# Kernel optimization log

Measured on AMD Instinct MI355X. Metric: run time of the kernel, lower is better.

Reference implementation:

```python
import jax, jax.numpy as jnp
import numpy as np

B, L, H, D = 1024, 32, 64, 2  # batch, lattice size, hiddenSize, inputDim (depth=1)
LOGP_FACTOR = 0.5


def setup_inputs() -> dict:
    key = jax.random.key(0)
    k0, k1, k2, k3 = jax.random.split(key, 4)
    x = jax.random.randint(k0, (B, L, L), 0, D, dtype=jnp.int32)
    # variance_scaling(fan_avg, uniform): limit = sqrt(3*scale / fan_avg)
    lim_in = float(np.sqrt(6.0 / (D + H)))
    lim_c = float(np.sqrt(3.0 / H))
    lim_out = float(np.sqrt(6.0 / (H + D)))
    Win = jax.random.uniform(k1, (D, H), jnp.float32, -lim_in, lim_in)
    Wc = jax.random.uniform(k2, (H, H), jnp.float32, -lim_c, lim_c)
    bc = jnp.zeros((H,), jnp.float32)
    Wout = jax.random.uniform(k3, (H, D), jnp.float32, -lim_out, lim_out)
    bout = jnp.zeros((D,), jnp.float32)
    return {"x": x, "Win": Win, "Wc": Wc, "bc": bc, "Wout": Wout, "bout": bout}


def reference(x, Win, Wc, bc, Wout, bout):
    Ldim = x.shape[-1]
    Hs = Wc.shape[0]
    Dd = Win.shape[0]
    # boustrophedon direction: +1 on even rows, -1 on odd rows
    dnp = np.ones(Ldim, dtype=np.int32)
    dnp[1::2] = -1
    direction = jnp.asarray(dnp)

    def flip_if(a, d):  # reverse_line: identity if d==1 else flip along axis 0
        return jnp.where(d == 1, a, jnp.flip(a, 0))

    def single(xs):  # xs: (L, L) int
        oh = jax.nn.one_hot(xs, Dd, dtype=Win.dtype)  # (L, L, D)

        def col_step(h, cin):
            cV, sH, sV = cin  # (H,), (D,), (D,)
            newR = sH + sV
            newH = jax.nn.elu((h + cV) @ Wc + bc + newR @ Win)  # RNNCell2D
            logits = jax.nn.log_softmax(newH @ Wout + bout)
            return newH, (newH, logits)

        def row_step(carry, row_in):
            prevH, prevOH = carry  # (L, H), (L, D)
            oh_row, d = row_in
            carryV = flip_if(prevH, d)
            stateV = flip_if(prevOH, d)
            stateH = jnp.concatenate(
                [jnp.zeros((1, Dd), oh.dtype), flip_if(oh_row, d)], axis=0)[:-1]
            _, (hs, logps) = jax.lax.scan(
                col_step, jnp.zeros((Hs,), Win.dtype), (carryV, stateH, stateV))
            logp_row = jnp.nan_to_num(
                jnp.sum(flip_if(logps, d) * oh_row, axis=-1), nan=-35.0)
            return (flip_if(hs, d), oh_row), logp_row

        init = (jnp.zeros((Ldim, Hs), Win.dtype), jnp.zeros((Ldim, Dd), Win.dtype))
        _, probs = jax.lax.scan(row_step, init, (oh, direction))
        return LOGP_FACTOR * jnp.sum(probs)

    return jax.vmap(single)(x)  # (B,) log-amplitudes
```

## Files before the change

### kernel.cpp

```cpp
#include <hip/hip_runtime.h>

#define LL 32
#define HH 64
#define PZS 68

typedef __attribute__((ext_vector_type(4))) float f32x4;

template <int CTRL>
__device__ __forceinline__ float dpp_add_step(float x) {
  int y = __builtin_amdgcn_update_dpp(0, __builtin_bit_cast(int, x), CTRL, 0xf, 0xf, true);
  return x + __builtin_bit_cast(float, y);
}

__device__ __forceinline__ float wave_sum64(float x) {
  x = dpp_add_step<0x111>(x);
  x = dpp_add_step<0x112>(x);
  x = dpp_add_step<0x114>(x);
  x = dpp_add_step<0x118>(x);
  x = dpp_add_step<0x142>(x);
  x = dpp_add_step<0x143>(x);
  return __builtin_bit_cast(float, __builtin_amdgcn_readlane(__builtin_bit_cast(int, x), 63));
}

__device__ __forceinline__ float rlbc(float v, int l) {
  return __builtin_bit_cast(float, __builtin_amdgcn_readlane(__builtin_bit_cast(int, v), l));
}

#define DECL_W(n) float w_##n = Wc[n * HH + lane];

#define MV4(i0, i1, i2, i3)                  \
  a0 = fmaf(rlbc(hv, i0), w_##i0, a0);       \
  a1 = fmaf(rlbc(hv, i1), w_##i1, a1);       \
  a2 = fmaf(rlbc(hv, i2), w_##i2, a2);       \
  a3 = fmaf(rlbc(hv, i3), w_##i3, a3);

#define PIN_ALL_W                                                              \
  asm volatile(""                                                              \
               : "+v"(w_0), "+v"(w_1), "+v"(w_2), "+v"(w_3), "+v"(w_4),       \
                 "+v"(w_5), "+v"(w_6), "+v"(w_7), "+v"(w_8), "+v"(w_9),       \
                 "+v"(w_10), "+v"(w_11), "+v"(w_12), "+v"(w_13), "+v"(w_14),  \
                 "+v"(w_15), "+v"(w_16), "+v"(w_17), "+v"(w_18), "+v"(w_19),  \
                 "+v"(w_20), "+v"(w_21), "+v"(w_22), "+v"(w_23), "+v"(w_24),  \
                 "+v"(w_25), "+v"(w_26), "+v"(w_27), "+v"(w_28), "+v"(w_29),  \
                 "+v"(w_30), "+v"(w_31), "+v"(w_32), "+v"(w_33), "+v"(w_34),  \
                 "+v"(w_35), "+v"(w_36), "+v"(w_37), "+v"(w_38), "+v"(w_39),  \
                 "+v"(w_40), "+v"(w_41), "+v"(w_42), "+v"(w_43), "+v"(w_44),  \
                 "+v"(w_45), "+v"(w_46), "+v"(w_47), "+v"(w_48), "+v"(w_49),  \
                 "+v"(w_50), "+v"(w_51), "+v"(w_52), "+v"(w_53), "+v"(w_54),  \
                 "+v"(w_55), "+v"(w_56), "+v"(w_57), "+v"(w_58), "+v"(w_59),  \
                 "+v"(w_60), "+v"(w_61), "+v"(w_62), "+v"(w_63), "+v"(win0),  \
                 "+v"(win1), "+v"(bcj), "+v"(dwout));

__global__ __launch_bounds__(64, 1) void rnn2d_kernel(
    const int* __restrict__ x, const float* __restrict__ Win,
    const float* __restrict__ Wc, const float* __restrict__ bc,
    const float* __restrict__ Wout, const float* __restrict__ bout,
    float* __restrict__ out) {
  const int lane = threadIdx.x;
  const int b = blockIdx.x;
  __shared__ float vrow[LL * HH];
  __shared__ float pz[LL * PZS];

  DECL_W(0)  DECL_W(1)  DECL_W(2)  DECL_W(3)  DECL_W(4)  DECL_W(5)  DECL_W(6)  DECL_W(7)
  DECL_W(8)  DECL_W(9)  DECL_W(10) DECL_W(11) DECL_W(12) DECL_W(13) DECL_W(14) DECL_W(15)
  DECL_W(16) DECL_W(17) DECL_W(18) DECL_W(19) DECL_W(20) DECL_W(21) DECL_W(22) DECL_W(23)
  DECL_W(24) DECL_W(25) DECL_W(26) DECL_W(27) DECL_W(28) DECL_W(29) DECL_W(30) DECL_W(31)
  DECL_W(32) DECL_W(33) DECL_W(34) DECL_W(35) DECL_W(36) DECL_W(37) DECL_W(38) DECL_W(39)
  DECL_W(40) DECL_W(41) DECL_W(42) DECL_W(43) DECL_W(44) DECL_W(45) DECL_W(46) DECL_W(47)
  DECL_W(48) DECL_W(49) DECL_W(50) DECL_W(51) DECL_W(52) DECL_W(53) DECL_W(54) DECL_W(55)
  DECL_W(56) DECL_W(57) DECL_W(58) DECL_W(59) DECL_W(60) DECL_W(61) DECL_W(62) DECL_W(63)

  float win0 = Win[lane];
  float win1 = Win[HH + lane];
  float bcj = bc[lane];
  float dwout = Wout[lane * 2 + 1] - Wout[lane * 2 + 0];
  const float dbout = bout[1] - bout[0];

#pragma unroll
  for (int c0 = 0; c0 < LL; ++c0) vrow[c0 * HH + lane] = 0.f;

  const int* xb = x + b * (LL * LL);
  unsigned prevmask = 0u;
  int spv = (lane < LL) ? xb[lane] : 0;
  float total_vec = 0.f;
  float hv = 0.f;

#pragma unroll 1
  for (int r = 0; r < LL; ++r) {
    const unsigned curmask =
        (unsigned)(__ballot(lane < LL && spv) & 0xffffffffull);
    if (r < LL - 1) spv = (lane < LL) ? xb[(r + 1) * LL + lane] : 0;

    const int odd = r & 1;
    const int d = odd ? -1 : 1;
    int c = odd ? (LL - 1) : 0;

#pragma unroll 2
    for (int k = 0; k < LL; ++k) {
      PIN_ALL_W

      const int cn = (c + d) & (LL - 1);
      const float vjn = vrow[cn * HH + lane];

      float a0 = 0.f, a1 = 0.f, a2 = 0.f, a3 = 0.f;
      MV4(0, 1, 2, 3)      MV4(4, 5, 6, 7)      MV4(8, 9, 10, 11)
      MV4(12, 13, 14, 15)  MV4(16, 17, 18, 19)  MV4(20, 21, 22, 23)
      MV4(24, 25, 26, 27)  MV4(28, 29, 30, 31)  MV4(32, 33, 34, 35)
      MV4(36, 37, 38, 39)  MV4(40, 41, 42, 43)  MV4(44, 45, 46, 47)
      MV4(48, 49, 50, 51)  MV4(52, 53, 54, 55)  MV4(56, 57, 58, 59)
      MV4(60, 61, 62, 63)

      float winc = 0.f;
      if (k > 0) {
        const unsigned sh = (curmask >> ((c - d) & 31)) & 1u;
        winc += sh ? win1 : win0;
      }
      if (r > 0) {
        const unsigned sv = (prevmask >> c) & 1u;
        winc += sv ? win1 : win0;
      }

      const float pre = ((a0 + a1) + (a2 + a3)) + bcj + winc;
      const float hnew = pre > 0.f ? pre : (__expf(pre) - 1.f);

      vrow[c * HH + lane] = hnew;
      pz[k * PZS + lane] = hnew * dwout;

      hv = hnew + ((k < LL - 1) ? vjn : 0.f);

      c = cn;
    }
    prevmask = curmask;

    {
      const int kk = lane & 31;
      const float* pzr = pz + kk * PZS;
      float s0 = 0.f, s1 = 0.f, s2 = 0.f, s3 = 0.f;
#pragma unroll
      for (int g = 0; g < 16; ++g) {
        const f32x4 v = *(const f32x4*)(pzr + 4 * g);
        s0 += v[0]; s1 += v[1]; s2 += v[2]; s3 += v[3];
      }
      const float dz = ((s0 + s1) + (s2 + s3)) + dbout;
      const int ck = odd ? (LL - 1 - kk) : kk;
      const unsigned spin = (curmask >> ck) & 1u;
      const float tt = __builtin_bit_cast(
          float, __builtin_bit_cast(unsigned, dz) ^ (spin << 31));
      float lpv = -(fmaxf(tt, 0.f) + __logf(1.f + __expf(-fabsf(tt))));
      lpv = (lpv == lpv) ? lpv : -35.0f;
      total_vec += (lane < LL) ? lpv : 0.f;
    }
  }

  const float grand = wave_sum64(total_vec);
  if (lane == 0) out[b] = 0.5f * grand;
}

extern "C" void kernel_launch(void* const* d_in, const int* in_sizes, int n_in,
                              void* d_out, int out_size, void* d_ws, size_t ws_size,
                              hipStream_t stream) {
  const int* x = (const int*)d_in[0];
  const float* Win = (const float*)d_in[1];
  const float* Wc = (const float*)d_in[2];
  const float* bc = (const float*)d_in[3];
  const float* Wout = (const float*)d_in[4];
  const float* bout = (const float*)d_in[5];
  float* out = (float*)d_out;
  rnn2d_kernel<<<dim3(out_size), dim3(64), 0, stream>>>(x, Win, Wc, bc, Wout, bout, out);
}
```

Before: 366.7 us.

## Process two batch samples per wavefront to interleave independent recurrences

Each 64-lane block now runs two batch elements together. Their matvec chains are interleaved so the register-resident Wc weights are shared, and two independent dependency chains hide readlane/FMA latency. The grid is halved to 512 blocks, leaving fewer waves on the 256-CU device, and the larger LDS footprint and register pressure could cause spills. Odd batch sizes would write out of bounds.

```diff
diff --git a/kernel.cpp b/kernel.cpp
--- a/kernel.cpp
+++ b/kernel.cpp
@@ -28,11 +28,15 @@
 
 #define DECL_W(n) float w_##n = Wc[n * HH + lane];
 
-#define MV4(i0, i1, i2, i3)                  \
-  a0 = fmaf(rlbc(hv, i0), w_##i0, a0);       \
-  a1 = fmaf(rlbc(hv, i1), w_##i1, a1);       \
-  a2 = fmaf(rlbc(hv, i2), w_##i2, a2);       \
-  a3 = fmaf(rlbc(hv, i3), w_##i3, a3);
+#define MV4D(i0, i1, i2, i3)                   \
+  a0A = fmaf(rlbc(hvA, i0), w_##i0, a0A);      \
+  a0B = fmaf(rlbc(hvB, i0), w_##i0, a0B);      \
+  a1A = fmaf(rlbc(hvA, i1), w_##i1, a1A);      \
+  a1B = fmaf(rlbc(hvB, i1), w_##i1, a1B);      \
+  a2A = fmaf(rlbc(hvA, i2), w_##i2, a2A);      \
+  a2B = fmaf(rlbc(hvB, i2), w_##i2, a2B);      \
+  a3A = fmaf(rlbc(hvA, i3), w_##i3, a3A);      \
+  a3B = fmaf(rlbc(hvB, i3), w_##i3, a3B);
 
 #define PIN_ALL_W                                                              \
   asm volatile(""                                                              \
@@ -57,9 +61,14 @@
     const float* __restrict__ Wout, const float* __restrict__ bout,
     float* __restrict__ out) {
   const int lane = threadIdx.x;
-  const int b = blockIdx.x;
-  __shared__ float vrow[LL * HH];
-  __shared__ float pz[LL * PZS];
+  const int b0 = blockIdx.x * 2;
+  const int b1 = b0 + 1;
+  __shared__ float vrow[2 * LL * HH];
+  __shared__ float pz[2 * LL * PZS];
+  float* vrowA = vrow;
+  float* vrowB = vrow + LL * HH;
+  float* pzA = pz;
+  float* pzB = pz + LL * PZS;
 
   DECL_W(0)  DECL_W(1)  DECL_W(2)  DECL_W(3)  DECL_W(4)  DECL_W(5)  DECL_W(6)  DECL_W(7)
   DECL_W(8)  DECL_W(9)  DECL_W(10) DECL_W(11) DECL_W(12) DECL_W(13) DECL_W(14) DECL_W(15)
@@ -77,19 +86,26 @@
   const float dbout = bout[1] - bout[0];
 
 #pragma unroll
-  for (int c0 = 0; c0 < LL; ++c0) vrow[c0 * HH + lane] = 0.f;
-
-  const int* xb = x + b * (LL * LL);
-  unsigned prevmask = 0u;
-  int spv = (lane < LL) ? xb[lane] : 0;
-  float total_vec = 0.f;
-  float hv = 0.f;
+  for (int c0 = 0; c0 < 2 * LL; ++c0) vrow[c0 * HH + lane] = 0.f;
+
+  const int* xb0 = x + b0 * (LL * LL);
+  const int* xb1 = x + b1 * (LL * LL);
+  unsigned prevmaskA = 0u, prevmaskB = 0u;
+  int spvA = (lane < LL) ? xb0[lane] : 0;
+  int spvB = (lane < LL) ? xb1[lane] : 0;
+  float totalA = 0.f, totalB = 0.f;
+  float hvA = 0.f, hvB = 0.f;
 
 #pragma unroll 1
   for (int r = 0; r < LL; ++r) {
-    const unsigned curmask =
-        (unsigned)(__ballot(lane < LL && spv) & 0xffffffffull);
-    if (r < LL - 1) spv = (lane < LL) ? xb[(r + 1) * LL + lane] : 0;
+    const unsigned curmaskA =
+        (unsigned)(__ballot(lane < LL && spvA) & 0xffffffffull);
+    const unsigned curmaskB =
+        (unsigned)(__ballot(lane < LL && spvB) & 0xffffffffull);
+    if (r < LL - 1) {
+      spvA = (lane < LL) ? xb0[(r + 1) * LL + lane] : 0;
+      spvB = (lane < LL) ? xb1[(r + 1) * LL + lane] : 0;
+    }
 
     const int odd = r & 1;
     const int d = odd ? -1 : 1;
@@ -100,60 +116,84 @@
       PIN_ALL_W
 
       const int cn = (c + d) & (LL - 1);
-      const float vjn = vrow[cn * HH + lane];
-
-      float a0 = 0.f, a1 = 0.f, a2 = 0.f, a3 = 0.f;
-      MV4(0, 1, 2, 3)      MV4(4, 5, 6, 7)      MV4(8, 9, 10, 11)
-      MV4(12, 13, 14, 15)  MV4(16, 17, 18, 19)  MV4(20, 21, 22, 23)
-      MV4(24, 25, 26, 27)  MV4(28, 29, 30, 31)  MV4(32, 33, 34, 35)
-      MV4(36, 37, 38, 39)  MV4(40, 41, 42, 43)  MV4(44, 45, 46, 47)
-      MV4(48, 49, 50, 51)  MV4(52, 53, 54, 55)  MV4(56, 57, 58, 59)
-      MV4(60, 61, 62, 63)
-
-      float winc = 0.f;
+      const float vjnA = vrowA[cn * HH + lane];
+      const float vjnB = vrowB[cn * HH + lane];
+
+      float a0A = 0.f, a1A = 0.f, a2A = 0.f, a3A = 0.f;
+      float a0B = 0.f, a1B = 0.f, a2B = 0.f, a3B = 0.f;
+      MV4D(0, 1, 2, 3)      MV4D(4, 5, 6, 7)      MV4D(8, 9, 10, 11)
+      MV4D(12, 13, 14, 15)  MV4D(16, 17, 18, 19)  MV4D(20, 21, 22, 23)
+      MV4D(24, 25, 26, 27)  MV4D(28, 29, 30, 31)  MV4D(32, 33, 34, 35)
+      MV4D(36, 37, 38, 39)  MV4D(40, 41, 42, 43)  MV4D(44, 45, 46, 47)
+      MV4D(48, 49, 50, 51)  MV4D(52, 53, 54, 55)  MV4D(56, 57, 58, 59)
+      MV4D(60, 61, 62, 63)
+
+      float wincA = 0.f, wincB = 0.f;
       if (k > 0) {
-        const unsigned sh = (curmask >> ((c - d) & 31)) & 1u;
-        winc += sh ? win1 : win0;
+        const int cp = (c - d) & 31;
+        wincA += ((curmaskA >> cp) & 1u) ? win1 : win0;
+        wincB += ((curmaskB >> cp) & 1u) ? win1 : win0;
       }
       if (r > 0) {
-        const unsigned sv = (prevmask >> c) & 1u;
-        winc += sv ? win1 : win0;
+        wincA += ((prevmaskA >> c) & 1u) ? win1 : win0;
+        wincB += ((prevmaskB >> c) & 1u) ? win1 : win0;
       }
 
-      const float pre = ((a0 + a1) + (a2 + a3)) + bcj + winc;
-      const float hnew = pre > 0.f ? pre : (__expf(pre) - 1.f);
-
-      vrow[c * HH + lane] = hnew;
-      pz[k * PZS + lane] = hnew * dwout;
-
-      hv = hnew + ((k < LL - 1) ? vjn : 0.f);
+      const float preA = ((a0A + a1A) + (a2A + a3A)) + bcj + wincA;
+      const float preB = ((a0B + a1B) + (a2B + a3B)) + bcj + wincB;
+      const float hnewA = preA > 0.f ? preA : (__expf(preA) - 1.f);
+      const float hnewB = preB > 0.f ? preB : (__expf(preB) - 1.f);
+
+      vrowA[c * HH + lane] = hnewA;
+      vrowB[c * HH + lane] = hnewB;
+      pzA[k * PZS + lane] = hnewA * dwout;
+      pzB[k * PZS + lane] = hnewB * dwout;
+
+      hvA = hnewA + ((k < LL - 1) ? vjnA : 0.f);
+      hvB = hnewB + ((k < LL - 1) ? vjnB : 0.f);
 
       c = cn;
     }
-    prevmask = curmask;
+    prevmaskA = curmaskA;
+    prevmaskB = curmaskB;
 
     {
       const int kk = lane & 31;
-      const float* pzr = pz + kk * PZS;
-      float s0 = 0.f, s1 = 0.f, s2 = 0.f, s3 = 0.f;
+      const float* pzrA = pzA + kk * PZS;
+      const float* pzrB = pzB + kk * PZS;
+      float s0A = 0.f, s1A = 0.f, s2A = 0.f, s3A = 0.f;
+      float s0B = 0.f, s1B = 0.f, s2B = 0.f, s3B = 0.f;
 #pragma unroll
       for (int g = 0; g < 16; ++g) {
-        const f32x4 v = *(const f32x4*)(pzr + 4 * g);
-        s0 += v[0]; s1 += v[1]; s2 += v[2]; s3 += v[3];
+        const f32x4 vA = *(const f32x4*)(pzrA + 4 * g);
+        const f32x4 vB = *(const f32x4*)(pzrB + 4 * g);
+        s0A += vA[0]; s1A += vA[1]; s2A += vA[2]; s3A += vA[3];
+        s0B += vB[0]; s1B += vB[1]; s2B += vB[2]; s3B += vB[3];
       }
-      const float dz = ((s0 + s1) + (s2 + s3)) + dbout;
+      const float dzA = ((s0A + s1A) + (s2A + s3A)) + dbout;
+      const float dzB = ((s0B + s1B) + (s2B + s3B)) + dbout;
       const int ck = odd ? (LL - 1 - kk) : kk;
-      const unsigned spin = (curmask >> ck) & 1u;
-      const float tt = __builtin_bit_cast(
-          float, __builtin_bit_cast(unsigned, dz) ^ (spin << 31));
-      float lpv = -(fmaxf(tt, 0.f) + __logf(1.f + __expf(-fabsf(tt))));
-      lpv = (lpv == lpv) ? lpv : -35.0f;
-      total_vec += (lane < LL) ? lpv : 0.f;
+      const unsigned spinA = (curmaskA >> ck) & 1u;
+      const unsigned spinB = (curmaskB >> ck) & 1u;
+      const float ttA = __builtin_bit_cast(
+          float, __builtin_bit_cast(unsigned, dzA) ^ (spinA << 31));
+      const float ttB = __builtin_bit_cast(
+          float, __builtin_bit_cast(unsigned, dzB) ^ (spinB << 31));
+      float lpvA = -(fmaxf(ttA, 0.f) + __logf(1.f + __expf(-fabsf(ttA))));
+      float lpvB = -(fmaxf(ttB, 0.f) + __logf(1.f + __expf(-fabsf(ttB))));
+      lpvA = (lpvA == lpvA) ? lpvA : -35.0f;
+      lpvB = (lpvB == lpvB) ? lpvB : -35.0f;
+      totalA += (lane < LL) ? lpvA : 0.f;
+      totalB += (lane < LL) ? lpvB : 0.f;
     }
   }
 
-  const float grand = wave_sum64(total_vec);
-  if (lane == 0) out[b] = 0.5f * grand;
+  const float grandA = wave_sum64(totalA);
+  const float grandB = wave_sum64(totalB);
+  if (lane == 0) {
+    out[b0] = 0.5f * grandA;
+    out[b1] = 0.5f * grandB;
+  }
 }
 
 extern "C" void kernel_launch(void* const* d_in, const int* in_sizes, int n_in,
@@ -166,5 +206,5 @@
   const float* Wout = (const float*)d_in[4];
   const float* bout = (const float*)d_in[5];
   float* out = (float*)d_out;
-  rnn2d_kernel<<<dim3(out_size), dim3(64), 0, stream>>>(x, Win, Wc, bc, Wout, bout, out);
-}
+  rnn2d_kernel<<<dim3((out_size + 1) / 2), dim3(64), 0, stream>>>(x, Win, Wc, bc, Wout, bout, out);
+}
```

After: 857.0 us. 2.34x slower.
